# Optimization experiments

Measured on AMD Instinct MI355X. Metric: run time of the kernel, lower is better.

Reference implementation:

```python
import jax, jax.numpy as jnp
import numpy as np
import math

B, Q_LEN, PAST, HID = 1, 1024, 3072, 4096
NH, NKV, HD = 32, 8, 128
KV_LEN = PAST + Q_LEN
ROPE_THETA = 10000.0


def setup_inputs() -> dict:
    key = jax.random.key(0)
    ks = jax.random.split(key, 8)
    s = 0.02
    hidden_states = jax.random.normal(ks[0], (B, Q_LEN, HID), jnp.float32)
    # additive causal mask with KV cache offset: query i attends keys j <= PAST + i
    i = jnp.arange(Q_LEN)[:, None]
    j = jnp.arange(KV_LEN)[None, :]
    attention_mask = jnp.where(j <= PAST + i, 0.0, -1e9).astype(jnp.float32)[None, None]
    position_ids = (jnp.arange(Q_LEN, dtype=jnp.int64) + PAST)[None, :]
    past_k = jax.random.normal(ks[1], (B, NKV, PAST, HD), jnp.float32)
    past_v = jax.random.normal(ks[2], (B, NKV, PAST, HD), jnp.float32)
    Wq = jax.random.normal(ks[3], (NH * HD, HID), jnp.float32) * s
    Wk = jax.random.normal(ks[4], (NKV * HD, HID), jnp.float32) * s
    Wv = jax.random.normal(ks[5], (NKV * HD, HID), jnp.float32) * s
    Wo = jax.random.normal(ks[6], (HID, NH * HD), jnp.float32) * s
    return {"hidden_states": hidden_states, "attention_mask": attention_mask,
            "position_ids": position_ids, "past_k": past_k, "past_v": past_v,
            "Wq": Wq, "Wk": Wk, "Wv": Wv, "Wo": Wo}


def _rope_tables(seq_len, head_dim, dtype):
    inv_freq = 1.0 / (ROPE_THETA ** (jnp.arange(0, head_dim, 2, dtype=jnp.float32) / head_dim))
    t = jnp.arange(seq_len, dtype=jnp.float32)
    freqs = jnp.outer(t, inv_freq)            # [seq, hd/2]
    emb = jnp.concatenate([freqs, freqs], -1)  # [seq, hd]
    return jnp.cos(emb).astype(dtype), jnp.sin(emb).astype(dtype)


def _rotate_half(x):
    x1, x2 = jnp.split(x, 2, axis=-1)
    return jnp.concatenate([-x2, x1], axis=-1)


def reference(hidden_states, attention_mask, position_ids, past_k, past_v, Wq, Wk, Wv, Wo):
    bsz, q_len, _ = hidden_states.shape
    q = (hidden_states @ Wq.T).reshape(bsz, q_len, NH, HD).transpose(0, 2, 1, 3)
    k = (hidden_states @ Wk.T).reshape(bsz, q_len, NKV, HD).transpose(0, 2, 1, 3)
    v = (hidden_states @ Wv.T).reshape(bsz, q_len, NKV, HD).transpose(0, 2, 1, 3)

    kv_seq_len = q_len + past_k.shape[2]
    cos_t, sin_t = _rope_tables(kv_seq_len, HD, q.dtype)
    cos = cos_t[position_ids][:, None]  # [b,1,q,hd]
    sin = sin_t[position_ids][:, None]
    q = q * cos + _rotate_half(q) * sin
    k = k * cos + _rotate_half(k) * sin

    k = jnp.concatenate([past_k, k], axis=2)  # [b,nkv,kv,hd]
    v = jnp.concatenate([past_v, v], axis=2)
    n_rep = NH // NKV
    k = jnp.repeat(k, n_rep, axis=1)  # GQA repeat_kv -> [b,nh,kv,hd]
    v = jnp.repeat(v, n_rep, axis=1)

    scores = jnp.einsum('bhqd,bhkd->bhqk', q, k) / math.sqrt(HD)
    scores = scores + attention_mask
    weights = jax.nn.softmax(scores.astype(jnp.float32), axis=-1).astype(q.dtype)
    attn = jnp.einsum('bhqk,bhkd->bhqd', weights, v)
    attn = attn.transpose(0, 2, 1, 3).reshape(bsz, q_len, NH * HD)
    return attn @ Wo.T
```

## Files before the change

### kernel.cpp

```cpp
#include <hip/hip_runtime.h>

#define QLEN 1024
#define PASTN 3072
#define KVLEN 4096
#define HIDN 4096
#define NHEAD 32
#define NKVH 8
#define HDIM 128
#define NQKVC 6144

typedef unsigned short u16;
typedef __bf16 bf16x8 __attribute__((ext_vector_type(8)));
typedef float f32x4 __attribute__((ext_vector_type(4)));
typedef float f32x16 __attribute__((ext_vector_type(16)));
typedef u16 us8 __attribute__((ext_vector_type(8)));
typedef u16 us4 __attribute__((ext_vector_type(4)));

__device__ __forceinline__ u16 f2bf(float x) {
  unsigned u = __builtin_bit_cast(unsigned, x);
  u += 0x7fffu + ((u >> 16) & 1u);
  return (u16)(u >> 16);
}
__device__ __forceinline__ float bf2f(u16 b) {
  return __builtin_bit_cast(float, (unsigned)b << 16);
}

#define GLL16(gp, lp) __builtin_amdgcn_global_load_lds( \
    (const __attribute__((address_space(1))) void*)(gp), \
    (__attribute__((address_space(3))) void*)(lp), 16, 0, 0)

__global__ __launch_bounds__(256) void cvt_kernel(const float* __restrict__ src,
                                                  u16* __restrict__ dst, int n) {
  int i = (blockIdx.x * 256 + threadIdx.x) * 4;
  if (i >= n) return;
  float4 f = *(const float4*)(src + i);
  ushort4 o = make_ushort4(f2bf(f.x), f2bf(f.y), f2bf(f.z), f2bf(f.w));
  *(ushort4*)(dst + i) = o;
}

__device__ __forceinline__ void storeC(float* p, float v) { *p = v; }
__device__ __forceinline__ void storeC(u16* p, float v) { *p = f2bf(v); }

template <typename CT>
__global__ __launch_bounds__(256) void gemm_bt(const u16* __restrict__ A,
                                               const u16* __restrict__ B,
                                               CT* __restrict__ C, int M, int N, int K) {
  __shared__ u16 Alds[2][64 * 32];
  __shared__ u16 Blds[2][128 * 32];
  const int tid = threadIdx.x, wid = tid >> 6, lane = tid & 63;
  const int m0 = blockIdx.y * 64, n0 = blockIdx.x * 128;
  const int wm = (wid >> 1) * 32, wn = (wid & 1) * 64;
  const int l15 = lane & 15, l4 = lane >> 4;
  const int srow = lane >> 2, sp = lane & 3;
  f32x4 acc[2][4] = {};
  auto stage = [&](int buf, int kt) {
    {
      const int r = wid * 16 + srow;
      GLL16(A + (size_t)(m0 + r) * K + kt + (sp ^ ((r >> 1) & 3)) * 8,
            &Alds[buf][wid * 512]);
    }
#pragma unroll
    for (int i = 0; i < 2; ++i) {
      const int c = wid * 2 + i;
      const int r = c * 16 + srow;
      GLL16(B + (size_t)(n0 + r) * K + kt + (sp ^ ((r >> 1) & 3)) * 8,
            &Blds[buf][c * 512]);
    }
  };
  stage(0, 0);
  __syncthreads();
  int cur = 0;
  for (int kt = 0; kt < K; kt += 32) {
    if (kt + 32 < K) stage(cur ^ 1, kt + 32);
    bf16x8 a[2], b[4];
#pragma unroll
    for (int i = 0; i < 2; ++i) {
      const int R = wm + i * 16 + l15;
      a[i] = *(const bf16x8*)&Alds[cur][R * 32 + (l4 ^ ((R >> 1) & 3)) * 8];
    }
#pragma unroll
    for (int j = 0; j < 4; ++j) {
      const int R = wn + j * 16 + l15;
      b[j] = *(const bf16x8*)&Blds[cur][R * 32 + (l4 ^ ((R >> 1) & 3)) * 8];
    }
#pragma unroll
    for (int i = 0; i < 2; ++i)
#pragma unroll
      for (int j = 0; j < 4; ++j)
        acc[i][j] = __builtin_amdgcn_mfma_f32_16x16x32_bf16(a[i], b[j], acc[i][j], 0, 0, 0);
    __syncthreads();
    cur ^= 1;
  }
#pragma unroll
  for (int i = 0; i < 2; ++i)
#pragma unroll
    for (int j = 0; j < 4; ++j) {
      int row = m0 + wm + i * 16 + l4 * 4;
      int col = n0 + wn + j * 16 + l15;
#pragma unroll
      for (int r = 0; r < 4; ++r) storeC(&C[(size_t)(row + r) * N + col], acc[i][j][r]);
    }
}

__global__ __launch_bounds__(256) void rope_q_kernel(const u16* __restrict__ qkv,
                                                     u16* __restrict__ qr) {
  int idx = blockIdx.x * 256 + threadIdx.x;
  int i = idx & 63, h = (idx >> 6) & 31, r = idx >> 11;
  float freq = __expf(-(float)i * (9.210340371976184f / 64.f));
  float angle = (float)(PASTN + r) * freq;
  float sn, cs;
  sincosf(angle, &sn, &cs);
  int base = r * NQKVC + h * HDIM + i;
  float x1 = bf2f(qkv[base]);
  float x2 = bf2f(qkv[base + 64]);
  int ob = r * HIDN + h * HDIM + i;
  qr[ob] = f2bf(x1 * cs - x2 * sn);
  qr[ob + 64] = f2bf(x2 * cs + x1 * sn);
}

__global__ __launch_bounds__(256) void repack_k_kernel(const float* __restrict__ past_k,
                                                       const u16* __restrict__ qkv,
                                                       u16* __restrict__ kb) {
  int idx = blockIdx.x * 256 + threadIdx.x;
  int d = idx & 127, kv = (idx >> 7) & 4095, hk = idx >> 19;
  float val;
  if (kv < PASTN) {
    val = past_k[((size_t)hk * PASTN + kv) * HDIM + d];
  } else {
    int r = kv - PASTN;
    float x = bf2f(qkv[(size_t)r * NQKVC + 4096 + hk * HDIM + d]);
    float xp = bf2f(qkv[(size_t)r * NQKVC + 4096 + hk * HDIM + (d ^ 64)]);
    int i = d & 63;
    float freq = __expf(-(float)i * (9.210340371976184f / 64.f));
    float angle = (float)(PASTN + r) * freq;
    float sn, cs;
    sincosf(angle, &sn, &cs);
    val = (d < 64) ? (x * cs - xp * sn) : (x * cs + xp * sn);
  }
  kb[idx] = f2bf(val);
}

__global__ __launch_bounds__(256) void repack_vt_kernel(const float* __restrict__ past_v,
                                                        const u16* __restrict__ qkv,
                                                        u16* __restrict__ vtb) {
  __shared__ u16 tile[32][136];
  int hk = blockIdx.y, kv0 = blockIdx.x * 32, tid = threadIdx.x;
  int j = tid >> 3, d0 = (tid & 7) * 16;
  if (kv0 < PASTN) {
    const float* src = past_v + ((size_t)hk * PASTN + kv0 + j) * HDIM + d0;
#pragma unroll
    for (int x = 0; x < 16; x += 4) {
      float4 f = *(const float4*)(src + x);
      tile[j][d0 + x] = f2bf(f.x);
      tile[j][d0 + x + 1] = f2bf(f.y);
      tile[j][d0 + x + 2] = f2bf(f.z);
      tile[j][d0 + x + 3] = f2bf(f.w);
    }
  } else {
    int r = kv0 - PASTN + j;
    const u16* src = qkv + (size_t)r * NQKVC + 5120 + hk * HDIM + d0;
    *(us8*)&tile[j][d0] = *(const us8*)src;
    *(us8*)&tile[j][d0 + 8] = *(const us8*)(src + 8);
  }
  __syncthreads();
  int d = tid >> 1, jb = (tid & 1) * 16;
  us8 o0, o1;
#pragma unroll
  for (int x = 0; x < 8; ++x) {
    o0[x] = tile[jb + x][d];
    o1[x] = tile[jb + 8 + x][d];
  }
  u16* dst = vtb + ((size_t)hk * HDIM + d) * KVLEN + kv0 + jb;
  *(us8*)dst = o0;
  *(us8*)(dst + 8) = o1;
}

__global__ __launch_bounds__(512) void attn_kernel(const u16* __restrict__ q,
                                                   const u16* __restrict__ kc,
                                                   const u16* __restrict__ vt,
                                                   float* __restrict__ opart,
                                                   float* __restrict__ mlbuf) {
  __shared__ u16 Klds[2][64 * 128];
  __shared__ u16 Vlds[2][128 * 64];
  const int tid = threadIdx.x, wid = tid >> 6, lane = tid & 63;
  const int l31 = lane & 31, hi = lane >> 5, l15 = lane & 15;
  const int h = blockIdx.y, hk = h >> 2;
  const int q0 = blockIdx.x * 256;
  const int z = blockIdx.z;
  const int pid = h * 4 + blockIdx.x;
  const int qrow = q0 + wid * 32 + l31;
  bf16x8 qf[8];
  {
    const u16* qp = q + (size_t)qrow * HIDN + h * HDIM + hi * 8;
#pragma unroll
    for (int dk = 0; dk < 8; ++dk) qf[dk] = *(const bf16x8*)(qp + dk * 16);
  }
  float m_run = -1e30f, l_run = 0.f;
  f32x16 oacc[4] = {};
  const u16* kbase = kc + (size_t)hk * KVLEN * HDIM;
  const u16* vbase = vt + (size_t)hk * HDIM * KVLEN;
  const int ntiles = (PASTN + q0 + 256) >> 6;
  const int half = ntiles >> 1;
  const int t0 = z ? half : 0, t1 = z ? ntiles : half;
  const float C = 0.12753102f;
  const int qpos = PASTN + qrow;
  auto stage = [&](int buf, int kv0) {
#pragma unroll
    for (int i = 0; i < 2; ++i) {
      const int w = wid * 2 + i;
      const int p = w * 4 + (lane >> 4);
      const int key = (p & 0x33) | ((p & 4) << 1) | ((p & 8) >> 1);
      const int sl = (lane & 15) ^ (p & 15);
      GLL16(kbase + (size_t)(kv0 + key) * HDIM + sl * 8, &Klds[buf][w * 512]);
    }
#pragma unroll
    for (int i = 0; i < 2; ++i) {
      const int w = wid * 2 + i;
      const int d = w * 8 + (lane >> 3);
      const int sl = (lane & 7) ^ ((lane >> 3) & 7);
      GLL16(vbase + (size_t)d * KVLEN + kv0 + sl * 8, &Vlds[buf][w * 512]);
    }
  };
  stage(0, t0 << 6);
  __syncthreads();
  int cur = 0;
  for (int t = t0; t < t1; ++t) {
    if (t + 1 < t1) stage(cur ^ 1, (t + 1) << 6);
    const int kv0 = t << 6;
    const u16* Kb = Klds[cur];
    const u16* Vb = Vlds[cur];
    f32x16 s[2] = {};
    __builtin_amdgcn_s_setprio(1);
#pragma unroll
    for (int tt = 0; tt < 2; ++tt)
#pragma unroll
      for (int dk = 0; dk < 8; ++dk) {
        const int idx = (tt * 32 + l31) * 128 + (((dk * 2 + hi) ^ l15) * 8);
        bf16x8 kf = *(const bf16x8*)&Kb[idx];
        s[tt] = __builtin_amdgcn_mfma_f32_32x32x16_bf16(kf, qf[dk], s[tt], 0, 0, 0);
      }
    __builtin_amdgcn_s_setprio(0);
    float pm = -1e30f;
    if (kv0 + 63 > PASTN + q0) {
#pragma unroll
      for (int tt = 0; tt < 2; ++tt)
#pragma unroll
        for (int reg = 0; reg < 16; ++reg) {
          const int key = kv0 + tt * 32 + (reg & 7) + 8 * hi + ((reg & 8) << 1);
          float v = s[tt][reg] * C;
          if (key > qpos) v = -1e30f;
          s[tt][reg] = v;
          pm = fmaxf(pm, v);
        }
    } else {
#pragma unroll
      for (int tt = 0; tt < 2; ++tt)
#pragma unroll
        for (int reg = 0; reg < 16; ++reg) {
          float v = s[tt][reg] * C;
          s[tt][reg] = v;
          pm = fmaxf(pm, v);
        }
    }
    pm = fmaxf(pm, __shfl_xor(pm, 32));
    if (!__all(pm <= m_run)) {
      const float mn = fmaxf(m_run, pm);
      const float corr = exp2f(m_run - mn);
      m_run = mn;
      l_run *= corr;
#pragma unroll
      for (int db = 0; db < 4; ++db)
#pragma unroll
        for (int r = 0; r < 16; ++r) oacc[db][r] *= corr;
    }
    float rs = 0.f;
#pragma unroll
    for (int tt = 0; tt < 2; ++tt)
#pragma unroll
      for (int reg = 0; reg < 16; ++reg) {
        const float p = exp2f(s[tt][reg] - m_run);
        s[tt][reg] = p;
        rs += p;
      }
    rs += __shfl_xor(rs, 32);
    l_run += rs;
    __builtin_amdgcn_s_setprio(1);
#pragma unroll
    for (int kc2 = 0; kc2 < 4; ++kc2) {
      bf16x8 pa;
#pragma unroll
      for (int j = 0; j < 8; ++j) pa[j] = (__bf16)s[kc2 >> 1][(kc2 & 1) * 8 + j];
#pragma unroll
      for (int db = 0; db < 4; ++db) {
        const int idx = (db * 32 + l31) * 64 + (((kc2 * 2 + hi) ^ (l31 & 7)) * 8);
        bf16x8 vf = *(const bf16x8*)&Vb[idx];
        oacc[db] = __builtin_amdgcn_mfma_f32_32x32x16_bf16(vf, pa, oacc[db], 0, 0, 0);
      }
    }
    __builtin_amdgcn_s_setprio(0);
    __syncthreads();
    cur ^= 1;
  }
  const int orow = wid * 32 + l31;
  float* op = opart + ((size_t)(z * 128 + pid) * 256 + orow) * 128;
#pragma unroll
  for (int db = 0; db < 4; ++db)
#pragma unroll
    for (int g = 0; g < 4; ++g) {
      f32x4 w4;
#pragma unroll
      for (int j = 0; j < 4; ++j) w4[j] = oacc[db][g * 4 + j];
      *(f32x4*)&op[db * 32 + g * 8 + hi * 4] = w4;
    }
  if (hi == 0) {
    float* mlp = mlbuf + ((size_t)(z * 128 + pid) * 256 + orow) * 2;
    mlp[0] = m_run;
    mlp[1] = l_run;
  }
}

__global__ __launch_bounds__(256) void attn_combine(const float* __restrict__ opart,
                                                    const float* __restrict__ mlbuf,
                                                    u16* __restrict__ o) {
  const int pid = blockIdx.x;
  const int h = pid >> 2, qt = pid & 3;
  const int q2 = threadIdx.x >> 2, dc = (threadIdx.x & 3) * 32;
#pragma unroll
  for (int b = 0; b < 4; ++b) {
    const int q = b * 64 + q2;
    const float* ml0 = mlbuf + ((size_t)pid * 256 + q) * 2;
    const float* ml1 = mlbuf + ((size_t)(128 + pid) * 256 + q) * 2;
    const float m0 = ml0[0], l0 = ml0[1], m1 = ml1[0], l1 = ml1[1];
    const float m = fmaxf(m0, m1);
    const float w0 = exp2f(m0 - m), w1 = exp2f(m1 - m);
    const float inv = 1.f / (w0 * l0 + w1 * l1);
    const float* O0 = opart + ((size_t)pid * 256 + q) * 128 + dc;
    const float* O1 = opart + ((size_t)(128 + pid) * 256 + q) * 128 + dc;
    u16* dst = o + (size_t)(qt * 256 + q) * HIDN + h * HDIM + dc;
#pragma unroll
    for (int x = 0; x < 8; ++x) {
      f32x4 a = *(const f32x4*)(O0 + x * 4);
      f32x4 bb = *(const f32x4*)(O1 + x * 4);
      us4 w4;
#pragma unroll
      for (int j = 0; j < 4; ++j) w4[j] = f2bf((a[j] * w0 + bb[j] * w1) * inv);
      *(us4*)(dst + x * 4) = w4;
    }
  }
}

extern "C" void kernel_launch(void* const* d_in, const int* in_sizes, int n_in,
                              void* d_out, int out_size, void* d_ws, size_t ws_size,
                              hipStream_t stream) {
  (void)in_sizes; (void)n_in; (void)out_size; (void)ws_size;
  const float* hidden = (const float*)d_in[0];
  const float* past_k = (const float*)d_in[3];
  const float* past_v = (const float*)d_in[4];
  const float* Wq = (const float*)d_in[5];
  const float* Wk = (const float*)d_in[6];
  const float* Wv = (const float*)d_in[7];
  const float* Wo = (const float*)d_in[8];
  float* out = (float*)d_out;

  char* w = (char*)d_ws;
  u16* hiddenb = (u16*)w; w += (size_t)QLEN * HIDN * 2;
  u16* wqkv    = (u16*)w; w += (size_t)NQKVC * HIDN * 2;
  u16* wo      = (u16*)w; w += (size_t)HIDN * HIDN * 2;
  u16* qkvraw  = (u16*)w; w += (size_t)QLEN * NQKVC * 2;
  u16* qrope   = (u16*)w; w += (size_t)QLEN * HIDN * 2;
  u16* kbuf    = (u16*)w; w += (size_t)NKVH * KVLEN * HDIM * 2;
  u16* vtbuf   = (u16*)w; w += (size_t)NKVH * HDIM * KVLEN * 2;
  u16* attnb   = (u16*)w; w += (size_t)QLEN * HIDN * 2;
  float* opart = (float*)wqkv;
  float* mlbuf = opart + (size_t)2 * 128 * 256 * 128;

  cvt_kernel<<<(QLEN * HIDN) / 1024, 256, 0, stream>>>(hidden, hiddenb, QLEN * HIDN);
  cvt_kernel<<<(NHEAD * HDIM * HIDN) / 1024, 256, 0, stream>>>(Wq, wqkv, NHEAD * HDIM * HIDN);
  cvt_kernel<<<(NKVH * HDIM * HIDN) / 1024, 256, 0, stream>>>(Wk, wqkv + (size_t)4096 * HIDN,
                                                              NKVH * HDIM * HIDN);
  cvt_kernel<<<(NKVH * HDIM * HIDN) / 1024, 256, 0, stream>>>(Wv, wqkv + (size_t)5120 * HIDN,
                                                              NKVH * HDIM * HIDN);
  cvt_kernel<<<(HIDN * HIDN) / 1024, 256, 0, stream>>>(Wo, wo, HIDN * HIDN);

  gemm_bt<u16><<<dim3(NQKVC / 128, QLEN / 64), 256, 0, stream>>>(hiddenb, wqkv, qkvraw,
                                                                 QLEN, NQKVC, HIDN);

  rope_q_kernel<<<(QLEN * NHEAD * 64) / 256, 256, 0, stream>>>(qkvraw, qrope);
  repack_k_kernel<<<(NKVH * KVLEN * HDIM) / 256, 256, 0, stream>>>(past_k, qkvraw, kbuf);
  repack_vt_kernel<<<dim3(KVLEN / 32, NKVH), 256, 0, stream>>>(past_v, qkvraw, vtbuf);

  attn_kernel<<<dim3(QLEN / 256, NHEAD, 2), 512, 0, stream>>>(qrope, kbuf, vtbuf,
                                                              opart, mlbuf);
  attn_combine<<<128, 256, 0, stream>>>(opart, mlbuf, attnb);

  gemm_bt<float><<<dim3(HIDN / 128, QLEN / 64), 256, 0, stream>>>(attnb, wo, out,
                                                                  QLEN, HIDN, HIDN);
}
```

Before: 344.6 us.

## Split attention KV range four ways and fuse input conversions into one launch

```diff
diff --git a/kernel.cpp b/kernel.cpp
--- a/kernel.cpp
+++ b/kernel.cpp
@@ -33,6 +33,26 @@
                                                   u16* __restrict__ dst, int n) {
   int i = (blockIdx.x * 256 + threadIdx.x) * 4;
   if (i >= n) return;
+  float4 f = *(const float4*)(src + i);
+  ushort4 o = make_ushort4(f2bf(f.x), f2bf(f.y), f2bf(f.z), f2bf(f.w));
+  *(ushort4*)(dst + i) = o;
+}
+
+__global__ __launch_bounds__(256) void cvt4_kernel(const float* __restrict__ hid,
+                                                   const float* __restrict__ wq,
+                                                   const float* __restrict__ wk,
+                                                   const float* __restrict__ wv,
+                                                   u16* __restrict__ hb,
+                                                   u16* __restrict__ wb) {
+  const int blk = blockIdx.x;
+  const float* src;
+  u16* dst;
+  int off;
+  if (blk < 4096)       { src = hid; dst = hb;                          off = blk; }
+  else if (blk < 20480) { src = wq;  dst = wb;                          off = blk - 4096; }
+  else if (blk < 24576) { src = wk;  dst = wb + (size_t)4096 * HIDN;    off = blk - 20480; }
+  else                  { src = wv;  dst = wb + (size_t)5120 * HIDN;    off = blk - 24576; }
+  const int i = off * 1024 + threadIdx.x * 4;
   float4 f = *(const float4*)(src + i);
   ushort4 o = make_ushort4(f2bf(f.x), f2bf(f.y), f2bf(f.z), f2bf(f.w));
   *(ushort4*)(dst + i) = o;
@@ -200,8 +220,8 @@
   const u16* kbase = kc + (size_t)hk * KVLEN * HDIM;
   const u16* vbase = vt + (size_t)hk * HDIM * KVLEN;
   const int ntiles = (PASTN + q0 + 256) >> 6;
-  const int half = ntiles >> 1;
-  const int t0 = z ? half : 0, t1 = z ? ntiles : half;
+  const int qtr = ntiles >> 2;
+  const int t0 = z * qtr, t1 = (z + 1) * qtr;
   const float C = 0.12753102f;
   const int qpos = PASTN + qrow;
   auto stage = [&](int buf, int kv0) {
@@ -328,22 +348,36 @@
 #pragma unroll
   for (int b = 0; b < 4; ++b) {
     const int q = b * 64 + q2;
-    const float* ml0 = mlbuf + ((size_t)pid * 256 + q) * 2;
-    const float* ml1 = mlbuf + ((size_t)(128 + pid) * 256 + q) * 2;
-    const float m0 = ml0[0], l0 = ml0[1], m1 = ml1[0], l1 = ml1[1];
-    const float m = fmaxf(m0, m1);
-    const float w0 = exp2f(m0 - m), w1 = exp2f(m1 - m);
-    const float inv = 1.f / (w0 * l0 + w1 * l1);
-    const float* O0 = opart + ((size_t)pid * 256 + q) * 128 + dc;
-    const float* O1 = opart + ((size_t)(128 + pid) * 256 + q) * 128 + dc;
+    float mz[4], lz[4];
+    float m = -1e30f;
+#pragma unroll
+    for (int zz = 0; zz < 4; ++zz) {
+      const float* ml = mlbuf + ((size_t)(zz * 128 + pid) * 256 + q) * 2;
+      mz[zz] = ml[0];
+      lz[zz] = ml[1];
+      m = fmaxf(m, mz[zz]);
+    }
+    float wz[4], l = 0.f;
+#pragma unroll
+    for (int zz = 0; zz < 4; ++zz) {
+      wz[zz] = exp2f(mz[zz] - m);
+      l += wz[zz] * lz[zz];
+    }
+    const float inv = 1.f / l;
     u16* dst = o + (size_t)(qt * 256 + q) * HIDN + h * HDIM + dc;
 #pragma unroll
     for (int x = 0; x < 8; ++x) {
-      f32x4 a = *(const f32x4*)(O0 + x * 4);
-      f32x4 bb = *(const f32x4*)(O1 + x * 4);
+      f32x4 acc = {0.f, 0.f, 0.f, 0.f};
+#pragma unroll
+      for (int zz = 0; zz < 4; ++zz) {
+        const float* O = opart + (((size_t)(zz * 128 + pid) * 256 + q) * 128) + dc;
+        f32x4 a = *(const f32x4*)(O + x * 4);
+#pragma unroll
+        for (int j = 0; j < 4; ++j) acc[j] += a[j] * wz[zz];
+      }
       us4 w4;
 #pragma unroll
-      for (int j = 0; j < 4; ++j) w4[j] = f2bf((a[j] * w0 + bb[j] * w1) * inv);
+      for (int j = 0; j < 4; ++j) w4[j] = f2bf(acc[j] * inv);
       *(us4*)(dst + x * 4) = w4;
     }
   }
@@ -371,16 +405,10 @@
   u16* kbuf    = (u16*)w; w += (size_t)NKVH * KVLEN * HDIM * 2;
   u16* vtbuf   = (u16*)w; w += (size_t)NKVH * HDIM * KVLEN * 2;
   u16* attnb   = (u16*)w; w += (size_t)QLEN * HIDN * 2;
-  float* opart = (float*)wqkv;
-  float* mlbuf = opart + (size_t)2 * 128 * 256 * 128;
-
-  cvt_kernel<<<(QLEN * HIDN) / 1024, 256, 0, stream>>>(hidden, hiddenb, QLEN * HIDN);
-  cvt_kernel<<<(NHEAD * HDIM * HIDN) / 1024, 256, 0, stream>>>(Wq, wqkv, NHEAD * HDIM * HIDN);
-  cvt_kernel<<<(NKVH * HDIM * HIDN) / 1024, 256, 0, stream>>>(Wk, wqkv + (size_t)4096 * HIDN,
-                                                              NKVH * HDIM * HIDN);
-  cvt_kernel<<<(NKVH * HDIM * HIDN) / 1024, 256, 0, stream>>>(Wv, wqkv + (size_t)5120 * HIDN,
-                                                              NKVH * HDIM * HIDN);
-  cvt_kernel<<<(HIDN * HIDN) / 1024, 256, 0, stream>>>(Wo, wo, HIDN * HIDN);
+  float* opart = (float*)d_ws;
+  float* mlbuf = opart + (size_t)4 * 128 * 256 * 128;
+
+  cvt4_kernel<<<28672, 256, 0, stream>>>(hidden, Wq, Wk, Wv, hiddenb, wqkv);
 
   gemm_bt<u16><<<dim3(NQKVC / 128, QLEN / 64), 256, 0, stream>>>(hiddenb, wqkv, qkvraw,
                                                                  QLEN, NQKVC, HIDN);
@@ -389,10 +417,11 @@
   repack_k_kernel<<<(NKVH * KVLEN * HDIM) / 256, 256, 0, stream>>>(past_k, qkvraw, kbuf);
   repack_vt_kernel<<<dim3(KVLEN / 32, NKVH), 256, 0, stream>>>(past_v, qkvraw, vtbuf);
 
-  attn_kernel<<<dim3(QLEN / 256, NHEAD, 2), 512, 0, stream>>>(qrope, kbuf, vtbuf,
+  attn_kernel<<<dim3(QLEN / 256, NHEAD, 4), 512, 0, stream>>>(qrope, kbuf, vtbuf,
                                                               opart, mlbuf);
   attn_combine<<<128, 256, 0, stream>>>(opart, mlbuf, attnb);
 
+  cvt_kernel<<<(HIDN * HIDN) / 1024, 256, 0, stream>>>(Wo, wo, HIDN * HIDN);
   gemm_bt<float><<<dim3(HIDN / 128, QLEN / 64), 256, 0, stream>>>(attnb, wo, out,
                                                                   QLEN, HIDN, HIDN);
 }
```

Result: slower. 354.8 us (+3.0%).

## Split-K the projection GEMMs, fuse weight conversions, fold softmax scale into Q

Applied to the files above, without the earlier changes.

```diff
diff --git a/kernel.cpp b/kernel.cpp
--- a/kernel.cpp
+++ b/kernel.cpp
@@ -29,13 +29,92 @@
     (const __attribute__((address_space(1))) void*)(gp), \
     (__attribute__((address_space(3))) void*)(lp), 16, 0, 0)
 
-__global__ __launch_bounds__(256) void cvt_kernel(const float* __restrict__ src,
-                                                  u16* __restrict__ dst, int n) {
-  int i = (blockIdx.x * 256 + threadIdx.x) * 4;
-  if (i >= n) return;
+__global__ __launch_bounds__(256) void cvt5_kernel(const float* __restrict__ hid,
+                                                   const float* __restrict__ wq,
+                                                   const float* __restrict__ wk,
+                                                   const float* __restrict__ wv,
+                                                   const float* __restrict__ woin,
+                                                   u16* __restrict__ hb,
+                                                   u16* __restrict__ wb,
+                                                   u16* __restrict__ wob) {
+  const int blk = blockIdx.x;
+  const float* src;
+  u16* dst;
+  int off;
+  if (blk < 4096)       { src = hid;  dst = hb;                       off = blk; }
+  else if (blk < 20480) { src = wq;   dst = wb;                       off = blk - 4096; }
+  else if (blk < 24576) { src = wk;   dst = wb + (size_t)4096 * HIDN; off = blk - 20480; }
+  else if (blk < 28672) { src = wv;   dst = wb + (size_t)5120 * HIDN; off = blk - 24576; }
+  else                  { src = woin; dst = wob;                      off = blk - 28672; }
+  const int i = off * 1024 + threadIdx.x * 4;
   float4 f = *(const float4*)(src + i);
   ushort4 o = make_ushort4(f2bf(f.x), f2bf(f.y), f2bf(f.z), f2bf(f.w));
   *(ushort4*)(dst + i) = o;
+}
+
+__global__ __launch_bounds__(256) void gemm_bt_split(const u16* __restrict__ A,
+                                                     const u16* __restrict__ B,
+                                                     float* __restrict__ P,
+                                                     int M, int N, int K, int Ks) {
+  __shared__ u16 Alds[2][64 * 32];
+  __shared__ u16 Blds[2][128 * 32];
+  const int tid = threadIdx.x, wid = tid >> 6, lane = tid & 63;
+  const int m0 = blockIdx.y * 64, n0 = blockIdx.x * 128;
+  const int z = blockIdx.z;
+  const u16* Az = A + (size_t)z * Ks;
+  const u16* Bz = B + (size_t)z * Ks;
+  float* Cz = P + (size_t)z * M * N;
+  const int wm = (wid >> 1) * 32, wn = (wid & 1) * 64;
+  const int l15 = lane & 15, l4 = lane >> 4;
+  const int srow = lane >> 2, sp = lane & 3;
+  f32x4 acc[2][4] = {};
+  auto stage = [&](int buf, int kt) {
+    {
+      const int r = wid * 16 + srow;
+      GLL16(Az + (size_t)(m0 + r) * K + kt + (sp ^ ((r >> 1) & 3)) * 8,
+            &Alds[buf][wid * 512]);
+    }
+#pragma unroll
+    for (int i = 0; i < 2; ++i) {
+      const int c = wid * 2 + i;
+      const int r = c * 16 + srow;
+      GLL16(Bz + (size_t)(n0 + r) * K + kt + (sp ^ ((r >> 1) & 3)) * 8,
+            &Blds[buf][c * 512]);
+    }
+  };
+  stage(0, 0);
+  __syncthreads();
+  int cur = 0;
+  for (int kt = 0; kt < Ks; kt += 32) {
+    if (kt + 32 < Ks) stage(cur ^ 1, kt + 32);
+    bf16x8 a[2], b[4];
+#pragma unroll
+    for (int i = 0; i < 2; ++i) {
+      const int R = wm + i * 16 + l15;
+      a[i] = *(const bf16x8*)&Alds[cur][R * 32 + (l4 ^ ((R >> 1) & 3)) * 8];
+    }
+#pragma unroll
+    for (int j = 0; j < 4; ++j) {
+      const int R = wn + j * 16 + l15;
+      b[j] = *(const bf16x8*)&Blds[cur][R * 32 + (l4 ^ ((R >> 1) & 3)) * 8];
+    }
+#pragma unroll
+    for (int i = 0; i < 2; ++i)
+#pragma unroll
+      for (int j = 0; j < 4; ++j)
+        acc[i][j] = __builtin_amdgcn_mfma_f32_16x16x32_bf16(a[i], b[j], acc[i][j], 0, 0, 0);
+    __syncthreads();
+    cur ^= 1;
+  }
+#pragma unroll
+  for (int i = 0; i < 2; ++i)
+#pragma unroll
+    for (int j = 0; j < 4; ++j) {
+      int row = m0 + wm + i * 16 + l4 * 4;
+      int col = n0 + wn + j * 16 + l15;
+#pragma unroll
+      for (int r = 0; r < 4; ++r) Cz[(size_t)(row + r) * N + col] = acc[i][j][r];
+    }
 }
 
 __device__ __forceinline__ void storeC(float* p, float v) { *p = v; }
@@ -102,8 +181,31 @@
     }
 }
 
+__global__ __launch_bounds__(256) void comb2_bf16(const float* __restrict__ P,
+                                                  u16* __restrict__ C, size_t MN) {
+  const size_t i = ((size_t)blockIdx.x * 256 + threadIdx.x) * 4;
+  f32x4 a = *(const f32x4*)(P + i);
+  f32x4 b = *(const f32x4*)(P + MN + i);
+  us4 o;
+#pragma unroll
+  for (int j = 0; j < 4; ++j) o[j] = f2bf(a[j] + b[j]);
+  *(us4*)(C + i) = o;
+}
+
+__global__ __launch_bounds__(256) void comb2_f32(const float* __restrict__ P,
+                                                 float* __restrict__ C, size_t MN) {
+  const size_t i = ((size_t)blockIdx.x * 256 + threadIdx.x) * 4;
+  f32x4 a = *(const f32x4*)(P + i);
+  f32x4 b = *(const f32x4*)(P + MN + i);
+  f32x4 o;
+#pragma unroll
+  for (int j = 0; j < 4; ++j) o[j] = a[j] + b[j];
+  *(f32x4*)(C + i) = o;
+}
+
 __global__ __launch_bounds__(256) void rope_q_kernel(const u16* __restrict__ qkv,
                                                      u16* __restrict__ qr) {
+  const float SC = 0.12753102f;
   int idx = blockIdx.x * 256 + threadIdx.x;
   int i = idx & 63, h = (idx >> 6) & 31, r = idx >> 11;
   float freq = __expf(-(float)i * (9.210340371976184f / 64.f));
@@ -114,8 +216,8 @@
   float x1 = bf2f(qkv[base]);
   float x2 = bf2f(qkv[base + 64]);
   int ob = r * HIDN + h * HDIM + i;
-  qr[ob] = f2bf(x1 * cs - x2 * sn);
-  qr[ob + 64] = f2bf(x2 * cs + x1 * sn);
+  qr[ob] = f2bf((x1 * cs - x2 * sn) * SC);
+  qr[ob + 64] = f2bf((x2 * cs + x1 * sn) * SC);
 }
 
 __global__ __launch_bounds__(256) void repack_k_kernel(const float* __restrict__ past_k,
@@ -202,7 +304,6 @@
   const int ntiles = (PASTN + q0 + 256) >> 6;
   const int half = ntiles >> 1;
   const int t0 = z ? half : 0, t1 = z ? ntiles : half;
-  const float C = 0.12753102f;
   const int qpos = PASTN + qrow;
   auto stage = [&](int buf, int kv0) {
 #pragma unroll
@@ -247,7 +348,7 @@
 #pragma unroll
         for (int reg = 0; reg < 16; ++reg) {
           const int key = kv0 + tt * 32 + (reg & 7) + 8 * hi + ((reg & 8) << 1);
-          float v = s[tt][reg] * C;
+          float v = s[tt][reg];
           if (key > qpos) v = -1e30f;
           s[tt][reg] = v;
           pm = fmaxf(pm, v);
@@ -256,11 +357,7 @@
 #pragma unroll
       for (int tt = 0; tt < 2; ++tt)
 #pragma unroll
-        for (int reg = 0; reg < 16; ++reg) {
-          float v = s[tt][reg] * C;
-          s[tt][reg] = v;
-          pm = fmaxf(pm, v);
-        }
+        for (int reg = 0; reg < 16; ++reg) pm = fmaxf(pm, s[tt][reg]);
     }
     pm = fmaxf(pm, __shfl_xor(pm, 32));
     if (!__all(pm <= m_run)) {
@@ -352,7 +449,7 @@
 extern "C" void kernel_launch(void* const* d_in, const int* in_sizes, int n_in,
                               void* d_out, int out_size, void* d_ws, size_t ws_size,
                               hipStream_t stream) {
-  (void)in_sizes; (void)n_in; (void)out_size; (void)ws_size;
+  (void)in_sizes; (void)n_in; (void)out_size;
   const float* hidden = (const float*)d_in[0];
   const float* past_k = (const float*)d_in[3];
   const float* past_v = (const float*)d_in[4];
@@ -371,19 +468,23 @@
   u16* kbuf    = (u16*)w; w += (size_t)NKVH * KVLEN * HDIM * 2;
   u16* vtbuf   = (u16*)w; w += (size_t)NKVH * HDIM * KVLEN * 2;
   u16* attnb   = (u16*)w; w += (size_t)QLEN * HIDN * 2;
+  float* gpart = (float*)w;
+  const size_t used = (size_t)(w - (char*)d_ws);
+  const size_t MN1 = (size_t)QLEN * NQKVC, MN2 = (size_t)QLEN * HIDN;
+  const bool canSplit = ws_size >= used + 2 * MN1 * sizeof(float);
   float* opart = (float*)wqkv;
   float* mlbuf = opart + (size_t)2 * 128 * 256 * 128;
 
-  cvt_kernel<<<(QLEN * HIDN) / 1024, 256, 0, stream>>>(hidden, hiddenb, QLEN * HIDN);
-  cvt_kernel<<<(NHEAD * HDIM * HIDN) / 1024, 256, 0, stream>>>(Wq, wqkv, NHEAD * HDIM * HIDN);
-  cvt_kernel<<<(NKVH * HDIM * HIDN) / 1024, 256, 0, stream>>>(Wk, wqkv + (size_t)4096 * HIDN,
-                                                              NKVH * HDIM * HIDN);
-  cvt_kernel<<<(NKVH * HDIM * HIDN) / 1024, 256, 0, stream>>>(Wv, wqkv + (size_t)5120 * HIDN,
-                                                              NKVH * HDIM * HIDN);
-  cvt_kernel<<<(HIDN * HIDN) / 1024, 256, 0, stream>>>(Wo, wo, HIDN * HIDN);
-
-  gemm_bt<u16><<<dim3(NQKVC / 128, QLEN / 64), 256, 0, stream>>>(hiddenb, wqkv, qkvraw,
-                                                                 QLEN, NQKVC, HIDN);
+  cvt5_kernel<<<45056, 256, 0, stream>>>(hidden, Wq, Wk, Wv, Wo, hiddenb, wqkv, wo);
+
+  if (canSplit) {
+    gemm_bt_split<<<dim3(NQKVC / 128, QLEN / 64, 2), 256, 0, stream>>>(
+        hiddenb, wqkv, gpart, QLEN, NQKVC, HIDN, HIDN / 2);
+    comb2_bf16<<<(int)(MN1 / 1024), 256, 0, stream>>>(gpart, qkvraw, MN1);
+  } else {
+    gemm_bt<u16><<<dim3(NQKVC / 128, QLEN / 64), 256, 0, stream>>>(hiddenb, wqkv, qkvraw,
+                                                                   QLEN, NQKVC, HIDN);
+  }
 
   rope_q_kernel<<<(QLEN * NHEAD * 64) / 256, 256, 0, stream>>>(qkvraw, qrope);
   repack_k_kernel<<<(NKVH * KVLEN * HDIM) / 256, 256, 0, stream>>>(past_k, qkvraw, kbuf);
@@ -393,6 +494,12 @@
                                                               opart, mlbuf);
   attn_combine<<<128, 256, 0, stream>>>(opart, mlbuf, attnb);
 
-  gemm_bt<float><<<dim3(HIDN / 128, QLEN / 64), 256, 0, stream>>>(attnb, wo, out,
-                                                                  QLEN, HIDN, HIDN);
-}
+  if (canSplit) {
+    gemm_bt_split<<<dim3(HIDN / 128, QLEN / 64, 2), 256, 0, stream>>>(
+        attnb, wo, gpart, QLEN, HIDN, HIDN, HIDN / 2);
+    comb2_f32<<<(int)(MN2 / 1024), 256, 0, stream>>>(gpart, out, MN2);
+  } else {
+    gemm_bt<float><<<dim3(HIDN / 128, QLEN / 64), 256, 0, stream>>>(attnb, wo, out,
+                                                                    QLEN, HIDN, HIDN);
+  }
+}
```

Result: no change. 339.7 us (-1.4%).
